# Optimization experiments

Measured on AMD Instinct MI355X. Metric: run time of the kernel, lower is better.

The kernel has to match this reference:

```python
import jax, jax.numpy as jnp
import numpy as np

N, D = 8192, 128
NOISEVAR = 1.0

def _softplusinverse(v):
    return np.log(1.0 - np.exp(-v)) + v

def setup_inputs() -> dict:
    key = jax.random.key(0)
    kx, kn = jax.random.split(key)
    x = jax.random.normal(kx, (N, D), dtype=jnp.float32)
    noise = jax.random.normal(kn, (N, D), dtype=jnp.float32)
    phi = jnp.asarray(_softplusinverse(NOISEVAR), dtype=jnp.float32)
    return {"x": x, "phi": phi, "noise": noise}

def reference(x, phi, noise):
    # x: [n, d] encoded features; phi: scalar noise param; noise: [n, d] i.i.d. N(0,1)
    n = x.shape[0]
    var = jax.nn.softplus(phi)
    # Pairwise squared L2 distances via Gram-matrix trick (same math as
    # norm(x_i - x_j)^2, avoids the [n, n, d] broadcast intermediate).
    sq = jnp.sum(x * x, axis=1)                                  # [n]
    d2 = jnp.maximum(sq[:, None] + sq[None, :] - 2.0 * (x @ x.T), 0.0)  # [n, n]
    kde_contribution = jnp.mean(jax.nn.logsumexp(-0.5 * d2 / var, axis=1))
    IXT_nats = jnp.log(jnp.float32(n)) - kde_contribution
    IXT = IXT_nats / jnp.log(jnp.float32(2.0))  # bits=True -> nats2bits
    out = x + var * noise                        # training=True noise injection
    return out, IXT
```

## Files before the change

kernel.cpp:

```cpp
#include <hip/hip_runtime.h>

#define N 8192
#define D 128
#define T64 64
#define NT64 (N / T64)

typedef __attribute__((ext_vector_type(4))) int intx4;
typedef unsigned long long u64;

static __device__ inline float softplus_of(const float* __restrict__ phi) {
    float p = phi[0];
    return (p > 20.f) ? p : log1pf(__expf(p));
}


__global__ __launch_bounds__(256) void k1_quant(
        const float* __restrict__ x,
        signed char* __restrict__ q8, int* __restrict__ sqv,
        float* __restrict__ rowsum) {
    int gid = blockIdx.x * 256 + threadIdx.x;
    int row = gid >> 4;
    int gc  = gid & 15;

    const float* xs = x + (size_t)row * D + gc * 8;
    float4 u = *(const float4*)xs, v = *(const float4*)(xs + 4);

    float f[8] = {u.x, u.y, u.z, u.w, v.x, v.y, v.z, v.w};
    u64 pack = 0;
    int s = 0;
    #pragma unroll
    for (int k = 0; k < 8; k++) {
        float c = fminf(fmaxf(f[k] * 16.f, -127.f), 127.f);
        int q = (int)rintf(c);
        s += q * q;
        pack |= ((u64)(q & 255)) << (8 * k);
    }
    *(u64*)&q8[(size_t)row * D + gc * 8] = pack;

    #pragma unroll
    for (int m = 1; m < 16; m <<= 1) s += __shfl_xor(s, m, 64);
    if (gc == 0) { sqv[row] = s; rowsum[row] = 0.f; }
}

__global__ __launch_bounds__(256, 3) void k2_gram(
        const signed char* __restrict__ q8, const float* __restrict__ phi,
        const int* __restrict__ sqv, float* __restrict__ rowsum) {
    const int w    = blockIdx.x * 4 + (threadIdx.x >> 6);
    const int lane = threadIdx.x & 63;
    const int lrow = lane & 15;
    const int quad = lane >> 4;

    const int cnt = (w < 2112) ? 3 : 2;
    int start     = (w < 2112) ? 3 * w : 2 * w + 2112;
    int ti = 0, rem = start, len = NT64;
    while (rem >= len) { rem -= len; ++ti; --len; }
    int tj = ti + rem;

    float var = softplus_of(phi);
    const float c2 = ((-0.5f / var) * 1.4426950408889634f) * (1.f / 256.f);
    const int Ts = (int)ceilf(30.f / (-c2));

    intx4 af[4][2], bf[4][2];
    int   sqi[4][4];
    int curTi = -1;

    #pragma unroll
    for (int nt = 0; nt < 4; nt++) {
        const signed char* br = q8 + (size_t)(tj * T64 + nt * 16 + lrow) * D + quad * 16;
        bf[nt][0] = *(const intx4*)br;
        bf[nt][1] = *(const intx4*)(br + 64);
    }

    for (int r = 0; r < cnt; ++r) {
        const int iB = ti * T64, jB = tj * T64;

        int sje[4];
        #pragma unroll
        for (int nt = 0; nt < 4; nt++)
            sje[nt] = sqv[jB + nt * 16 + lrow];

        if (ti != curTi) {
            #pragma unroll
            for (int mt = 0; mt < 4; mt++) {
                const signed char* ar =
                    q8 + (size_t)(iB + mt * 16 + lrow) * D + quad * 16;
                af[mt][0] = *(const intx4*)ar;
                af[mt][1] = *(const intx4*)(ar + 64);
            }
            #pragma unroll
            for (int mt = 0; mt < 4; mt++)
                #pragma unroll
                for (int reg = 0; reg < 4; reg++)
                    sqi[mt][reg] = sqv[iB + mt * 16 + quad * 4 + reg];
            curTi = ti;
        }

        int nti = ti, ntj = tj + 1;
        if (ntj == NT64) { ++nti; ntj = nti; }
        const bool more = (r + 1 < cnt);

        #pragma unroll
        for (int nt = 0; nt < 4; nt++) {
            intx4 acc[4] = {};
            #pragma unroll
            for (int kk = 0; kk < 2; kk++)
                #pragma unroll
                for (int mt = 0; mt < 4; mt++)
                    acc[mt] = __builtin_amdgcn_mfma_i32_16x16x64_i8(
                        af[mt][kk], bf[nt][kk], acc[mt], 0, 0, 0);

            if (more) {
                const signed char* br =
                    q8 + (size_t)(ntj * T64 + nt * 16 + lrow) * D + quad * 16;
                bf[nt][0] = *(const intx4*)br;
                bf[nt][1] = *(const intx4*)(br + 64);
            }

            const int sj = sje[nt];
            int mn = 0x7fffffff;
            #pragma unroll
            for (int mt = 0; mt < 4; mt++)
                #pragma unroll
                for (int reg = 0; reg < 4; reg++) {
                    int d2s = sqi[mt][reg] + sj - (acc[mt][reg] << 1);
                    mn = min(mn, d2s);
                }

            if (__any(mn < Ts)) {
                float colv = 0.f;
                #pragma unroll
                for (int mt = 0; mt < 4; mt++)
                    #pragma unroll
                    for (int reg = 0; reg < 4; reg++) {
                        int d2s = sqi[mt][reg] + sj - (acc[mt][reg] << 1);
                        float p = __builtin_amdgcn_exp2f((float)d2s * c2);
                        colv += p;
                        float rv = p;
                        rv += __shfl_xor(rv, 1, 64);
                        rv += __shfl_xor(rv, 2, 64);
                        rv += __shfl_xor(rv, 4, 64);
                        rv += __shfl_xor(rv, 8, 64);
                        if (lrow == 0)
                            atomicAdd(&rowsum[iB + mt * 16 + quad * 4 + reg], rv);
                    }
                if (ti != tj) {
                    colv += __shfl_xor(colv, 16, 64);
                    colv += __shfl_xor(colv, 32, 64);
                    if (quad == 0)
                        atomicAdd(&rowsum[jB + nt * 16 + lrow], colv);
                }
            }
        }

        ti = nti; tj = ntj;
    }
}

__global__ __launch_bounds__(1024) void k3_final(
        const float* __restrict__ rowsum, float* __restrict__ out_ixt) {
    __shared__ float red[16];
    int t = threadIdx.x;
    float local = 0.f;
    for (int i = t; i < N; i += 1024) local += logf(rowsum[i]);
    #pragma unroll
    for (int m = 1; m < 64; m <<= 1) local += __shfl_xor(local, m, 64);
    if ((t & 63) == 0) red[t >> 6] = local;
    __syncthreads();
    if (t < 16) {
        float v = red[t];
        #pragma unroll
        for (int m = 1; m < 16; m <<= 1) v += __shfl_xor(v, m, 64);
        if (t == 0) {
            float kde = v / (float)N;
            out_ixt[0] = (logf((float)N) - kde) * 1.4426950408889634f;
        }
    }
}

__global__ __launch_bounds__(256) void k4_out(
        const float* __restrict__ x, const float* __restrict__ phi,
        const float* __restrict__ noise, float* __restrict__ out) {
    int gid = blockIdx.x * 256 + threadIdx.x;
    float var = softplus_of(phi);
    const float* xs = x     + (size_t)gid * 8;
    const float* ns = noise + (size_t)gid * 8;
    float4 u  = *(const float4*)xs, v  = *(const float4*)(xs + 4);
    float4 nu = *(const float4*)ns, nv = *(const float4*)(ns + 4);
    float4 o0, o1;
    o0.x = u.x + var * nu.x; o0.y = u.y + var * nu.y;
    o0.z = u.z + var * nu.z; o0.w = u.w + var * nu.w;
    o1.x = v.x + var * nv.x; o1.y = v.y + var * nv.y;
    o1.z = v.z + var * nv.z; o1.w = v.w + var * nv.w;
    float* od = out + (size_t)gid * 8;
    *(float4*)od = o0; *(float4*)(od + 4) = o1;
}

extern "C" void kernel_launch(void* const* d_in, const int* in_sizes, int n_in,
                              void* d_out, int out_size, void* d_ws, size_t ws_size,
                              hipStream_t stream) {
    const float* x     = (const float*)d_in[0];
    const float* phi   = (const float*)d_in[1];
    const float* noise = (const float*)d_in[2];
    float* out = (float*)d_out;

    signed char* q8  = (signed char*)out;
    int*   sqv    = (int*)(out + (size_t)N * D / 4);
    float* rowsum = (float*)(sqv + N);

    k1_quant<<<(N * 16) / 256, 256, 0, stream>>>(x, q8, sqv, rowsum);
    k2_gram<<<768, 256, 0, stream>>>(q8, phi, sqv, rowsum);
    k3_final<<<1, 1024, 0, stream>>>(rowsum, out + (size_t)N * D);
    k4_out<<<(N * D / 8) / 256, 256, 0, stream>>>(x, phi, noise, out);
}
```

Measured before the change: 93.60 us.

## Fuse quantize, gram, reduction and output into one cooperative kernel

Replaces the four separate launches with a single cooperative kernel of 512 blocks that uses grid-wide syncs between the quantize, tiled int8 Gram/logsumexp, log-reduction and noise-output phases. Work per wave in the Gram phase is rebalanced to 4-5 tile pairs to fit the smaller persistent grid, and the final reduction becomes atomics plus a last-phase finalize. The aim is to remove launch gaps and the single-block final kernel, at the cost of grid-sync overhead and lower occupancy (launch bounds 256,2). It falls back to the old multi-kernel path if the cooperative launch fails.

```diff
diff --git a/kernel.cpp b/kernel.cpp
--- a/kernel.cpp
+++ b/kernel.cpp
@@ -1,9 +1,13 @@
 #include <hip/hip_runtime.h>
+#include <hip/hip_cooperative_groups.h>
+
+namespace cg = cooperative_groups;
 
 #define N 8192
 #define D 128
 #define T64 64
 #define NT64 (N / T64)
+#define GBLK 512
 
 typedef __attribute__((ext_vector_type(4))) int intx4;
 typedef unsigned long long u64;
@@ -13,6 +17,179 @@
     return (p > 20.f) ? p : log1pf(__expf(p));
 }
 
+__global__ __launch_bounds__(256, 2) void fused(
+        const float* __restrict__ x, const float* __restrict__ phi,
+        const float* __restrict__ noise, float* out) {
+    signed char* q8   = (signed char*)out;
+    int*         sqv    = (int*)(out + (size_t)N * D / 4);
+    float*       rowsum = (float*)(sqv + N);
+    float*       ixt    = out + (size_t)N * D;
+
+    cg::grid_group grid = cg::this_grid();
+    const int tid = threadIdx.x;
+    const int gid = blockIdx.x * 256 + tid;
+    const float var = softplus_of(phi);
+
+    {
+        int row = gid >> 4, gc = gid & 15;
+        const float* xs = x + (size_t)row * D + gc * 8;
+        float4 u = *(const float4*)xs, v = *(const float4*)(xs + 4);
+        float f[8] = {u.x, u.y, u.z, u.w, v.x, v.y, v.z, v.w};
+        u64 pack = 0;
+        int s = 0;
+        #pragma unroll
+        for (int k = 0; k < 8; k++) {
+            float c = fminf(fmaxf(f[k] * 16.f, -127.f), 127.f);
+            int q = (int)rintf(c);
+            s += q * q;
+            pack |= ((u64)(q & 255)) << (8 * k);
+        }
+        *(u64*)&q8[(size_t)row * D + gc * 8] = pack;
+        #pragma unroll
+        for (int m = 1; m < 16; m <<= 1) s += __shfl_xor(s, m, 64);
+        if (gc == 0) { sqv[row] = s; rowsum[row] = 0.f; }
+        if (gid == 0) ixt[0] = 0.f;
+    }
+    grid.sync();
+
+    {
+        const int w    = blockIdx.x * 4 + (tid >> 6);
+        const int lane = tid & 63;
+        const int lrow = lane & 15;
+        const int quad = lane >> 4;
+
+        const int cnt = (w < 64) ? 5 : 4;
+        int start     = (w < 64) ? 5 * w : 4 * w + 64;
+        int ti = 0, rem = start, len = NT64;
+        while (rem >= len) { rem -= len; ++ti; --len; }
+        int tj = ti + rem;
+
+        const float c2 = ((-0.5f / var) * 1.4426950408889634f) * (1.f / 256.f);
+        const int Ts = (int)ceilf(30.f / (-c2));
+
+        intx4 af[4][2], bf[4][2];
+        int   sqi[4][4];
+        int curTi = -1;
+
+        #pragma unroll
+        for (int nt = 0; nt < 4; nt++) {
+            const signed char* br = q8 + (size_t)(tj * T64 + nt * 16 + lrow) * D + quad * 16;
+            bf[nt][0] = *(const intx4*)br;
+            bf[nt][1] = *(const intx4*)(br + 64);
+        }
+
+        for (int r = 0; r < cnt; ++r) {
+            const int iB = ti * T64, jB = tj * T64;
+
+            int sje[4];
+            #pragma unroll
+            for (int nt = 0; nt < 4; nt++)
+                sje[nt] = sqv[jB + nt * 16 + lrow];
+
+            if (ti != curTi) {
+                #pragma unroll
+                for (int mt = 0; mt < 4; mt++) {
+                    const signed char* ar =
+                        q8 + (size_t)(iB + mt * 16 + lrow) * D + quad * 16;
+                    af[mt][0] = *(const intx4*)ar;
+                    af[mt][1] = *(const intx4*)(ar + 64);
+                }
+                #pragma unroll
+                for (int mt = 0; mt < 4; mt++)
+                    #pragma unroll
+                    for (int reg = 0; reg < 4; reg++)
+                        sqi[mt][reg] = sqv[iB + mt * 16 + quad * 4 + reg];
+                curTi = ti;
+            }
+
+            int nti = ti, ntj = tj + 1;
+            if (ntj == NT64) { ++nti; ntj = nti; }
+            const bool more = (r + 1 < cnt);
+
+            #pragma unroll
+            for (int nt = 0; nt < 4; nt++) {
+                intx4 acc[4] = {};
+                #pragma unroll
+                for (int kk = 0; kk < 2; kk++)
+                    #pragma unroll
+                    for (int mt = 0; mt < 4; mt++)
+                        acc[mt] = __builtin_amdgcn_mfma_i32_16x16x64_i8(
+                            af[mt][kk], bf[nt][kk], acc[mt], 0, 0, 0);
+
+                if (more) {
+                    const signed char* br =
+                        q8 + (size_t)(ntj * T64 + nt * 16 + lrow) * D + quad * 16;
+                    bf[nt][0] = *(const intx4*)br;
+                    bf[nt][1] = *(const intx4*)(br + 64);
+                }
+
+                const int sj = sje[nt];
+                int mn = 0x7fffffff;
+                #pragma unroll
+                for (int mt = 0; mt < 4; mt++)
+                    #pragma unroll
+                    for (int reg = 0; reg < 4; reg++) {
+                        int d2s = sqi[mt][reg] + sj - (acc[mt][reg] << 1);
+                        mn = min(mn, d2s);
+                    }
+
+                if (__any(mn < Ts)) {
+                    float colv = 0.f;
+                    #pragma unroll
+                    for (int mt = 0; mt < 4; mt++)
+                        #pragma unroll
+                        for (int reg = 0; reg < 4; reg++) {
+                            int d2s = sqi[mt][reg] + sj - (acc[mt][reg] << 1);
+                            float p = __builtin_amdgcn_exp2f((float)d2s * c2);
+                            colv += p;
+                            float rv = p;
+                            rv += __shfl_xor(rv, 1, 64);
+                            rv += __shfl_xor(rv, 2, 64);
+                            rv += __shfl_xor(rv, 4, 64);
+                            rv += __shfl_xor(rv, 8, 64);
+                            if (lrow == 0)
+                                atomicAdd(&rowsum[iB + mt * 16 + quad * 4 + reg], rv);
+                        }
+                    if (ti != tj) {
+                        colv += __shfl_xor(colv, 16, 64);
+                        colv += __shfl_xor(colv, 32, 64);
+                        if (quad == 0)
+                            atomicAdd(&rowsum[jB + nt * 16 + lrow], colv);
+                    }
+                }
+            }
+
+            ti = nti; tj = ntj;
+        }
+    }
+    grid.sync();
+
+    if (gid < N) {
+        float l = logf(rowsum[gid]);
+        #pragma unroll
+        for (int m = 1; m < 64; m <<= 1) l += __shfl_xor(l, m, 64);
+        if ((tid & 63) == 0) atomicAdd(ixt, l);
+    }
+    grid.sync();
+
+    {
+        const float* xs = x     + (size_t)gid * 8;
+        const float* ns = noise + (size_t)gid * 8;
+        float4 u  = *(const float4*)xs, v  = *(const float4*)(xs + 4);
+        float4 nu = *(const float4*)ns, nv = *(const float4*)(ns + 4);
+        float4 o0, o1;
+        o0.x = u.x + var * nu.x; o0.y = u.y + var * nu.y;
+        o0.z = u.z + var * nu.z; o0.w = u.w + var * nu.w;
+        o1.x = v.x + var * nv.x; o1.y = v.y + var * nv.y;
+        o1.z = v.z + var * nv.z; o1.w = v.w + var * nv.w;
+        if (gid == 0) {
+            float S = ixt[0];
+            ixt[0] = (logf((float)N) - S / (float)N) * 1.4426950408889634f;
+        }
+        float* od = out + (size_t)gid * 8;
+        *(float4*)od = o0; *(float4*)(od + 4) = o1;
+    }
+}
 
 __global__ __launch_bounds__(256) void k1_quant(
         const float* __restrict__ x,
@@ -21,10 +198,8 @@
     int gid = blockIdx.x * 256 + threadIdx.x;
     int row = gid >> 4;
     int gc  = gid & 15;
-
     const float* xs = x + (size_t)row * D + gc * 8;
     float4 u = *(const float4*)xs, v = *(const float4*)(xs + 4);
-
     float f[8] = {u.x, u.y, u.z, u.w, v.x, v.y, v.z, v.w};
     u64 pack = 0;
     int s = 0;
@@ -36,7 +211,6 @@
         pack |= ((u64)(q & 255)) << (8 * k);
     }
     *(u64*)&q8[(size_t)row * D + gc * 8] = pack;
-
     #pragma unroll
     for (int m = 1; m < 16; m <<= 1) s += __shfl_xor(s, m, 64);
     if (gc == 0) { sqv[row] = s; rowsum[row] = 0.f; }
@@ -49,36 +223,29 @@
     const int lane = threadIdx.x & 63;
     const int lrow = lane & 15;
     const int quad = lane >> 4;
-
     const int cnt = (w < 2112) ? 3 : 2;
     int start     = (w < 2112) ? 3 * w : 2 * w + 2112;
     int ti = 0, rem = start, len = NT64;
     while (rem >= len) { rem -= len; ++ti; --len; }
     int tj = ti + rem;
-
     float var = softplus_of(phi);
     const float c2 = ((-0.5f / var) * 1.4426950408889634f) * (1.f / 256.f);
     const int Ts = (int)ceilf(30.f / (-c2));
-
     intx4 af[4][2], bf[4][2];
     int   sqi[4][4];
     int curTi = -1;
-
     #pragma unroll
     for (int nt = 0; nt < 4; nt++) {
         const signed char* br = q8 + (size_t)(tj * T64 + nt * 16 + lrow) * D + quad * 16;
         bf[nt][0] = *(const intx4*)br;
         bf[nt][1] = *(const intx4*)(br + 64);
     }
-
     for (int r = 0; r < cnt; ++r) {
         const int iB = ti * T64, jB = tj * T64;
-
         int sje[4];
         #pragma unroll
         for (int nt = 0; nt < 4; nt++)
             sje[nt] = sqv[jB + nt * 16 + lrow];
-
         if (ti != curTi) {
             #pragma unroll
             for (int mt = 0; mt < 4; mt++) {
@@ -94,11 +261,9 @@
                     sqi[mt][reg] = sqv[iB + mt * 16 + quad * 4 + reg];
             curTi = ti;
         }
-
         int nti = ti, ntj = tj + 1;
         if (ntj == NT64) { ++nti; ntj = nti; }
         const bool more = (r + 1 < cnt);
-
         #pragma unroll
         for (int nt = 0; nt < 4; nt++) {
             intx4 acc[4] = {};
@@ -108,14 +273,12 @@
                 for (int mt = 0; mt < 4; mt++)
                     acc[mt] = __builtin_amdgcn_mfma_i32_16x16x64_i8(
                         af[mt][kk], bf[nt][kk], acc[mt], 0, 0, 0);
-
             if (more) {
                 const signed char* br =
                     q8 + (size_t)(ntj * T64 + nt * 16 + lrow) * D + quad * 16;
                 bf[nt][0] = *(const intx4*)br;
                 bf[nt][1] = *(const intx4*)(br + 64);
             }
-
             const int sj = sje[nt];
             int mn = 0x7fffffff;
             #pragma unroll
@@ -125,7 +288,6 @@
                     int d2s = sqi[mt][reg] + sj - (acc[mt][reg] << 1);
                     mn = min(mn, d2s);
                 }
-
             if (__any(mn < Ts)) {
                 float colv = 0.f;
                 #pragma unroll
@@ -151,7 +313,6 @@
                 }
             }
         }
-
         ti = nti; tj = ntj;
     }
 }
@@ -203,12 +364,17 @@
     const float* noise = (const float*)d_in[2];
     float* out = (float*)d_out;
 
-    signed char* q8  = (signed char*)out;
-    int*   sqv    = (int*)(out + (size_t)N * D / 4);
-    float* rowsum = (float*)(sqv + N);
-
-    k1_quant<<<(N * 16) / 256, 256, 0, stream>>>(x, q8, sqv, rowsum);
-    k2_gram<<<768, 256, 0, stream>>>(q8, phi, sqv, rowsum);
-    k3_final<<<1, 1024, 0, stream>>>(rowsum, out + (size_t)N * D);
-    k4_out<<<(N * D / 8) / 256, 256, 0, stream>>>(x, phi, noise, out);
-}
+    void* args[] = {(void*)&x, (void*)&phi, (void*)&noise, (void*)&out};
+    hipError_t e = hipLaunchCooperativeKernel(
+        reinterpret_cast<void*>(fused), dim3(GBLK), dim3(256), args, 0, stream);
+    if (e != hipSuccess) {
+        (void)hipGetLastError();
+        signed char* q8  = (signed char*)out;
+        int*   sqv    = (int*)(out + (size_t)N * D / 4);
+        float* rowsum = (float*)(sqv + N);
+        k1_quant<<<(N * 16) / 256, 256, 0, stream>>>(x, q8, sqv, rowsum);
+        k2_gram<<<768, 256, 0, stream>>>(q8, phi, sqv, rowsum);
+        k3_final<<<1, 1024, 0, stream>>>(rowsum, out + (size_t)N * D);
+        k4_out<<<(N * D / 8) / 256, 256, 0, stream>>>(x, phi, noise, out);
+    }
+}
```

Result: slower. 256.6 us (+174.1%).

## Fuse output noise into prep, finalize in gram kernel, add cheaper tile skip test

Applied to the files above, without the earlier changes.

The noise-injection output for rows beyond the scratch prefix is now written by the quantization kernel, and the final out kernel only covers the prefix rows used as scratch. The separate logsumexp finalize kernel is folded into the gram kernel through a last-block-done atomic counter. Each 16-row group's minimum squared norm is precomputed, so the gram kernel can reject a tile using only a max over the accumulators before computing full distances. This removes one launch and some redundant x reads, at the cost of a grid-wide counter and extra scratch writes.

```diff
diff --git a/kernel.cpp b/kernel.cpp
--- a/kernel.cpp
+++ b/kernel.cpp
@@ -4,6 +4,8 @@
 #define D 128
 #define T64 64
 #define NT64 (N / T64)
+#define PREFIX 2192
+#define K2BLK 768
 
 typedef __attribute__((ext_vector_type(4))) int intx4;
 typedef unsigned long long u64;
@@ -14,11 +16,15 @@
 }
 
 
-__global__ __launch_bounds__(256) void k1_quant(
-        const float* __restrict__ x,
+__global__ __launch_bounds__(256) void k1_prep(
+        const float* __restrict__ x, const float* __restrict__ phi,
+        const float* __restrict__ noise, float* __restrict__ out,
         signed char* __restrict__ q8, int* __restrict__ sqv,
-        float* __restrict__ rowsum) {
-    int gid = blockIdx.x * 256 + threadIdx.x;
+        float* __restrict__ rowsum, int* __restrict__ sqmin16,
+        int* __restrict__ counter) {
+    __shared__ int smin[16];
+    int tid = threadIdx.x;
+    int gid = blockIdx.x * 256 + tid;
     int row = gid >> 4;
     int gc  = gid & 15;
 
@@ -39,14 +45,40 @@
 
     #pragma unroll
     for (int m = 1; m < 16; m <<= 1) s += __shfl_xor(s, m, 64);
-    if (gc == 0) { sqv[row] = s; rowsum[row] = 0.f; }
+    if (gc == 0) { sqv[row] = s; rowsum[row] = 0.f; smin[tid >> 4] = s; }
+    if (gid == 0) counter[0] = 0;
+    __syncthreads();
+    if (tid == 0) {
+        int m = smin[0];
+        #pragma unroll
+        for (int k = 1; k < 16; k++) m = min(m, smin[k]);
+        sqmin16[blockIdx.x] = m;
+    }
+
+    if (row >= PREFIX) {
+        float var = softplus_of(phi);
+        const float* ns = noise + (size_t)row * D + gc * 8;
+        float4 nu = *(const float4*)ns, nv = *(const float4*)(ns + 4);
+        float4 o0, o1;
+        o0.x = u.x + var * nu.x; o0.y = u.y + var * nu.y;
+        o0.z = u.z + var * nu.z; o0.w = u.w + var * nu.w;
+        o1.x = v.x + var * nv.x; o1.y = v.y + var * nv.y;
+        o1.z = v.z + var * nv.z; o1.w = v.w + var * nv.w;
+        float* od = out + (size_t)row * D + gc * 8;
+        *(float4*)od = o0; *(float4*)(od + 4) = o1;
+    }
 }
 
 __global__ __launch_bounds__(256, 3) void k2_gram(
         const signed char* __restrict__ q8, const float* __restrict__ phi,
-        const int* __restrict__ sqv, float* __restrict__ rowsum) {
-    const int w    = blockIdx.x * 4 + (threadIdx.x >> 6);
-    const int lane = threadIdx.x & 63;
+        const int* __restrict__ sqv, float* __restrict__ rowsum,
+        const int* __restrict__ sqmin16, int* __restrict__ counter,
+        float* __restrict__ out_ixt) {
+    __shared__ float red[4];
+    __shared__ int sh_last;
+    const int tid  = threadIdx.x;
+    const int w    = blockIdx.x * 4 + (tid >> 6);
+    const int lane = tid & 63;
     const int lrow = lane & 15;
     const int quad = lane >> 4;
 
@@ -62,6 +94,7 @@
 
     intx4 af[4][2], bf[4][2];
     int   sqi[4][4];
+    int   sqiMin = 0;
     int curTi = -1;
 
     #pragma unroll
@@ -74,10 +107,12 @@
     for (int r = 0; r < cnt; ++r) {
         const int iB = ti * T64, jB = tj * T64;
 
-        int sje[4];
-        #pragma unroll
-        for (int nt = 0; nt < 4; nt++)
+        int sje[4], sjm[4];
+        #pragma unroll
+        for (int nt = 0; nt < 4; nt++) {
             sje[nt] = sqv[jB + nt * 16 + lrow];
+            sjm[nt] = sqmin16[tj * 4 + nt];
+        }
 
         if (ti != curTi) {
             #pragma unroll
@@ -92,6 +127,8 @@
                 #pragma unroll
                 for (int reg = 0; reg < 4; reg++)
                     sqi[mt][reg] = sqv[iB + mt * 16 + quad * 4 + reg];
+            sqiMin = min(min(sqmin16[ti * 4 + 0], sqmin16[ti * 4 + 1]),
+                         min(sqmin16[ti * 4 + 2], sqmin16[ti * 4 + 3]));
             curTi = ti;
         }
 
@@ -116,62 +153,77 @@
                 bf[nt][1] = *(const intx4*)(br + 64);
             }
 
-            const int sj = sje[nt];
-            int mn = 0x7fffffff;
+            int mx = acc[0][0];
             #pragma unroll
             for (int mt = 0; mt < 4; mt++)
                 #pragma unroll
-                for (int reg = 0; reg < 4; reg++) {
-                    int d2s = sqi[mt][reg] + sj - (acc[mt][reg] << 1);
-                    mn = min(mn, d2s);
-                }
-
-            if (__any(mn < Ts)) {
-                float colv = 0.f;
+                for (int reg = 0; reg < 4; reg++)
+                    mx = max(mx, acc[mt][reg]);
+            const int Sthr = sqiMin + sjm[nt] - Ts;
+
+            if (__any((mx << 1) > Sthr)) {
+                const int sj = sje[nt];
+                int mn = 0x7fffffff;
                 #pragma unroll
                 for (int mt = 0; mt < 4; mt++)
                     #pragma unroll
                     for (int reg = 0; reg < 4; reg++) {
                         int d2s = sqi[mt][reg] + sj - (acc[mt][reg] << 1);
-                        float p = __builtin_amdgcn_exp2f((float)d2s * c2);
-                        colv += p;
-                        float rv = p;
-                        rv += __shfl_xor(rv, 1, 64);
-                        rv += __shfl_xor(rv, 2, 64);
-                        rv += __shfl_xor(rv, 4, 64);
-                        rv += __shfl_xor(rv, 8, 64);
-                        if (lrow == 0)
-                            atomicAdd(&rowsum[iB + mt * 16 + quad * 4 + reg], rv);
+                        mn = min(mn, d2s);
                     }
-                if (ti != tj) {
-                    colv += __shfl_xor(colv, 16, 64);
-                    colv += __shfl_xor(colv, 32, 64);
-                    if (quad == 0)
-                        atomicAdd(&rowsum[jB + nt * 16 + lrow], colv);
+
+                if (__any(mn < Ts)) {
+                    float colv = 0.f;
+                    #pragma unroll
+                    for (int mt = 0; mt < 4; mt++)
+                        #pragma unroll
+                        for (int reg = 0; reg < 4; reg++) {
+                            int d2s = sqi[mt][reg] + sj - (acc[mt][reg] << 1);
+                            float p = __builtin_amdgcn_exp2f((float)d2s * c2);
+                            colv += p;
+                            float rv = p;
+                            rv += __shfl_xor(rv, 1, 64);
+                            rv += __shfl_xor(rv, 2, 64);
+                            rv += __shfl_xor(rv, 4, 64);
+                            rv += __shfl_xor(rv, 8, 64);
+                            if (lrow == 0)
+                                atomicAdd(&rowsum[iB + mt * 16 + quad * 4 + reg], rv);
+                        }
+                    if (ti != tj) {
+                        colv += __shfl_xor(colv, 16, 64);
+                        colv += __shfl_xor(colv, 32, 64);
+                        if (quad == 0)
+                            atomicAdd(&rowsum[jB + nt * 16 + lrow], colv);
+                    }
                 }
             }
         }
 
         ti = nti; tj = ntj;
     }
-}
-
-__global__ __launch_bounds__(1024) void k3_final(
-        const float* __restrict__ rowsum, float* __restrict__ out_ixt) {
-    __shared__ float red[16];
-    int t = threadIdx.x;
-    float local = 0.f;
-    for (int i = t; i < N; i += 1024) local += logf(rowsum[i]);
-    #pragma unroll
-    for (int m = 1; m < 64; m <<= 1) local += __shfl_xor(local, m, 64);
-    if ((t & 63) == 0) red[t >> 6] = local;
+
     __syncthreads();
-    if (t < 16) {
-        float v = red[t];
-        #pragma unroll
-        for (int m = 1; m < 16; m <<= 1) v += __shfl_xor(v, m, 64);
-        if (t == 0) {
-            float kde = v / (float)N;
+    if (tid == 0) {
+        __threadfence();
+        int old = __hip_atomic_fetch_add(counter, 1, __ATOMIC_ACQ_REL,
+                                         __HIP_MEMORY_SCOPE_AGENT);
+        sh_last = (old == K2BLK - 1);
+    }
+    __syncthreads();
+    if (sh_last) {
+        float l = 0.f;
+        for (int i = tid; i < N; i += 256) {
+            float rv = __hip_atomic_load(&rowsum[i], __ATOMIC_RELAXED,
+                                         __HIP_MEMORY_SCOPE_AGENT);
+            l += logf(rv);
+        }
+        #pragma unroll
+        for (int m = 1; m < 64; m <<= 1) l += __shfl_xor(l, m, 64);
+        if ((tid & 63) == 0) red[tid >> 6] = l;
+        __syncthreads();
+        if (tid == 0) {
+            float S = red[0] + red[1] + red[2] + red[3];
+            float kde = S / (float)N;
             out_ixt[0] = (logf((float)N) - kde) * 1.4426950408889634f;
         }
     }
@@ -203,12 +255,15 @@
     const float* noise = (const float*)d_in[2];
     float* out = (float*)d_out;
 
-    signed char* q8  = (signed char*)out;
-    int*   sqv    = (int*)(out + (size_t)N * D / 4);
-    float* rowsum = (float*)(sqv + N);
-
-    k1_quant<<<(N * 16) / 256, 256, 0, stream>>>(x, q8, sqv, rowsum);
-    k2_gram<<<768, 256, 0, stream>>>(q8, phi, sqv, rowsum);
-    k3_final<<<1, 1024, 0, stream>>>(rowsum, out + (size_t)N * D);
-    k4_out<<<(N * D / 8) / 256, 256, 0, stream>>>(x, phi, noise, out);
-}
+    signed char* q8     = (signed char*)out;
+    int*         sqv     = (int*)(out + (size_t)N * D / 4);
+    float*       rowsum  = (float*)(sqv + N);
+    int*         sqmin16 = (int*)(rowsum + N);
+    int*         counter = sqmin16 + (N / 16);
+
+    k1_prep<<<(N * 16) / 256, 256, 0, stream>>>(
+        x, phi, noise, out, q8, sqv, rowsum, sqmin16, counter);
+    k2_gram<<<K2BLK, 256, 0, stream>>>(
+        q8, phi, sqv, rowsum, sqmin16, counter, out + (size_t)N * D);
+    k4_out<<<(PREFIX * 16) / 256, 256, 0, stream>>>(x, phi, noise, out);
+}
```

Measured after the change: 111.8 us. +19.5%, slower.

## Fuse noise output into quant pass, one tile per wave, merge final reduction

Applied to the files above, without the earlier changes.

The quantisation kernel now also writes x + var*noise for rows at or above 2176, which lie past the scratch region held in the output buffer. The final output kernel writes the remaining rows and, in its first block, also does the logsumexp reduction, so the separate reduce launch goes away. The Gram kernel gives each wave a single 64x64 tile pair, found with a closed-form triangular index, instead of looping over 2-3 tiles, and raises the launch-bounds occupancy hint from 3 to 4. The aim is to cut launches and the duplicate reads of x, at the cost of losing B-fragment prefetch reuse across tiles and launching more waves.

```diff
diff --git a/kernel.cpp b/kernel.cpp
--- a/kernel.cpp
+++ b/kernel.cpp
@@ -4,6 +4,9 @@
 #define D 128
 #define T64 64
 #define NT64 (N / T64)
+#define NPAIR (NT64 * (NT64 + 1) / 2)
+#define PREFIX 2176
+#define TBASE(t) ((t) * NT64 - ((t) * ((t) - 1)) / 2)
 
 typedef __attribute__((ext_vector_type(4))) int intx4;
 typedef unsigned long long u64;
@@ -14,11 +17,13 @@
 }
 
 
-__global__ __launch_bounds__(256) void k1_quant(
-        const float* __restrict__ x,
+__global__ __launch_bounds__(256) void k1_prep(
+        const float* __restrict__ x, const float* __restrict__ phi,
+        const float* __restrict__ noise, float* __restrict__ out,
         signed char* __restrict__ q8, int* __restrict__ sqv,
         float* __restrict__ rowsum) {
-    int gid = blockIdx.x * 256 + threadIdx.x;
+    int tid = threadIdx.x;
+    int gid = blockIdx.x * 256 + tid;
     int row = gid >> 4;
     int gc  = gid & 15;
 
@@ -40,159 +45,163 @@
     #pragma unroll
     for (int m = 1; m < 16; m <<= 1) s += __shfl_xor(s, m, 64);
     if (gc == 0) { sqv[row] = s; rowsum[row] = 0.f; }
-}
-
-__global__ __launch_bounds__(256, 3) void k2_gram(
+
+    if (row >= PREFIX) {
+        float var = softplus_of(phi);
+        const float* ns = noise + (size_t)row * D + gc * 8;
+        float4 nu = *(const float4*)ns, nv = *(const float4*)(ns + 4);
+        float4 o0, o1;
+        o0.x = u.x + var * nu.x; o0.y = u.y + var * nu.y;
+        o0.z = u.z + var * nu.z; o0.w = u.w + var * nu.w;
+        o1.x = v.x + var * nv.x; o1.y = v.y + var * nv.y;
+        o1.z = v.z + var * nv.z; o1.w = v.w + var * nv.w;
+        float* od = out + (size_t)row * D + gc * 8;
+        *(float4*)od = o0; *(float4*)(od + 4) = o1;
+    }
+}
+
+__global__ __launch_bounds__(256, 4) void k2_gram(
         const signed char* __restrict__ q8, const float* __restrict__ phi,
         const int* __restrict__ sqv, float* __restrict__ rowsum) {
-    const int w    = blockIdx.x * 4 + (threadIdx.x >> 6);
-    const int lane = threadIdx.x & 63;
+    const int tid  = threadIdx.x;
+    const int w    = blockIdx.x * 4 + (tid >> 6);
+    const int lane = tid & 63;
     const int lrow = lane & 15;
     const int quad = lane >> 4;
 
-    const int cnt = (w < 2112) ? 3 : 2;
-    int start     = (w < 2112) ? 3 * w : 2 * w + 2112;
-    int ti = 0, rem = start, len = NT64;
-    while (rem >= len) { rem -= len; ++ti; --len; }
-    int tj = ti + rem;
-
-    float var = softplus_of(phi);
+    const float fm = (float)(2 * NT64 + 1);
+    int ti = (int)((fm - sqrtf(fm * fm - 8.0f * (float)w)) * 0.5f);
+    while (TBASE(ti + 1) <= w) ++ti;
+    while (TBASE(ti) > w) --ti;
+    const int tj = ti + (w - TBASE(ti));
+
+    const float var = softplus_of(phi);
     const float c2 = ((-0.5f / var) * 1.4426950408889634f) * (1.f / 256.f);
     const int Ts = (int)ceilf(30.f / (-c2));
 
-    intx4 af[4][2], bf[4][2];
-    int   sqi[4][4];
-    int curTi = -1;
-
+    const int iB = ti * T64, jB = tj * T64;
+
+    intx4 af[4][2], bf[4][2], sqi[4];
+    int   sje[4];
+    #pragma unroll
+    for (int mt = 0; mt < 4; mt++) {
+        const signed char* ar = q8 + (size_t)(iB + mt * 16 + lrow) * D + quad * 16;
+        af[mt][0] = *(const intx4*)ar;
+        af[mt][1] = *(const intx4*)(ar + 64);
+    }
     #pragma unroll
     for (int nt = 0; nt < 4; nt++) {
-        const signed char* br = q8 + (size_t)(tj * T64 + nt * 16 + lrow) * D + quad * 16;
+        const signed char* br = q8 + (size_t)(jB + nt * 16 + lrow) * D + quad * 16;
         bf[nt][0] = *(const intx4*)br;
         bf[nt][1] = *(const intx4*)(br + 64);
     }
-
-    for (int r = 0; r < cnt; ++r) {
-        const int iB = ti * T64, jB = tj * T64;
-
-        int sje[4];
-        #pragma unroll
-        for (int nt = 0; nt < 4; nt++)
-            sje[nt] = sqv[jB + nt * 16 + lrow];
-
-        if (ti != curTi) {
-            #pragma unroll
-            for (int mt = 0; mt < 4; mt++) {
-                const signed char* ar =
-                    q8 + (size_t)(iB + mt * 16 + lrow) * D + quad * 16;
-                af[mt][0] = *(const intx4*)ar;
-                af[mt][1] = *(const intx4*)(ar + 64);
-            }
+    #pragma unroll
+    for (int mt = 0; mt < 4; mt++)
+        sqi[mt] = *(const intx4*)&sqv[iB + mt * 16 + quad * 4];
+    #pragma unroll
+    for (int nt = 0; nt < 4; nt++)
+        sje[nt] = sqv[jB + nt * 16 + lrow];
+
+    #pragma unroll
+    for (int nt = 0; nt < 4; nt++) {
+        intx4 acc[4] = {};
+        #pragma unroll
+        for (int kk = 0; kk < 2; kk++)
             #pragma unroll
             for (int mt = 0; mt < 4; mt++)
-                #pragma unroll
-                for (int reg = 0; reg < 4; reg++)
-                    sqi[mt][reg] = sqv[iB + mt * 16 + quad * 4 + reg];
-            curTi = ti;
-        }
-
-        int nti = ti, ntj = tj + 1;
-        if (ntj == NT64) { ++nti; ntj = nti; }
-        const bool more = (r + 1 < cnt);
-
-        #pragma unroll
-        for (int nt = 0; nt < 4; nt++) {
-            intx4 acc[4] = {};
+                acc[mt] = __builtin_amdgcn_mfma_i32_16x16x64_i8(
+                    af[mt][kk], bf[nt][kk], acc[mt], 0, 0, 0);
+
+        const int sj = sje[nt];
+        int mn = 0x7fffffff;
+        #pragma unroll
+        for (int mt = 0; mt < 4; mt++)
             #pragma unroll
-            for (int kk = 0; kk < 2; kk++)
-                #pragma unroll
-                for (int mt = 0; mt < 4; mt++)
-                    acc[mt] = __builtin_amdgcn_mfma_i32_16x16x64_i8(
-                        af[mt][kk], bf[nt][kk], acc[mt], 0, 0, 0);
-
-            if (more) {
-                const signed char* br =
-                    q8 + (size_t)(ntj * T64 + nt * 16 + lrow) * D + quad * 16;
-                bf[nt][0] = *(const intx4*)br;
-                bf[nt][1] = *(const intx4*)(br + 64);
+            for (int reg = 0; reg < 4; reg++) {
+                int d2s = sqi[mt][reg] + sj - (acc[mt][reg] << 1);
+                mn = min(mn, d2s);
             }
 
-            const int sj = sje[nt];
-            int mn = 0x7fffffff;
+        if (__any(mn < Ts)) {
+            float colv = 0.f;
             #pragma unroll
             for (int mt = 0; mt < 4; mt++)
                 #pragma unroll
                 for (int reg = 0; reg < 4; reg++) {
                     int d2s = sqi[mt][reg] + sj - (acc[mt][reg] << 1);
-                    mn = min(mn, d2s);
+                    float p = __builtin_amdgcn_exp2f((float)d2s * c2);
+                    colv += p;
+                    float rv = p;
+                    rv += __shfl_xor(rv, 1, 64);
+                    rv += __shfl_xor(rv, 2, 64);
+                    rv += __shfl_xor(rv, 4, 64);
+                    rv += __shfl_xor(rv, 8, 64);
+                    if (lrow == 0)
+                        atomicAdd(&rowsum[iB + mt * 16 + quad * 4 + reg], rv);
                 }
-
-            if (__any(mn < Ts)) {
-                float colv = 0.f;
-                #pragma unroll
-                for (int mt = 0; mt < 4; mt++)
-                    #pragma unroll
-                    for (int reg = 0; reg < 4; reg++) {
-                        int d2s = sqi[mt][reg] + sj - (acc[mt][reg] << 1);
-                        float p = __builtin_amdgcn_exp2f((float)d2s * c2);
-                        colv += p;
-                        float rv = p;
-                        rv += __shfl_xor(rv, 1, 64);
-                        rv += __shfl_xor(rv, 2, 64);
-                        rv += __shfl_xor(rv, 4, 64);
-                        rv += __shfl_xor(rv, 8, 64);
-                        if (lrow == 0)
-                            atomicAdd(&rowsum[iB + mt * 16 + quad * 4 + reg], rv);
-                    }
-                if (ti != tj) {
-                    colv += __shfl_xor(colv, 16, 64);
-                    colv += __shfl_xor(colv, 32, 64);
-                    if (quad == 0)
-                        atomicAdd(&rowsum[jB + nt * 16 + lrow], colv);
-                }
+            if (ti != tj) {
+                colv += __shfl_xor(colv, 16, 64);
+                colv += __shfl_xor(colv, 32, 64);
+                if (quad == 0)
+                    atomicAdd(&rowsum[jB + nt * 16 + lrow], colv);
             }
         }
-
-        ti = nti; tj = ntj;
-    }
-}
-
-__global__ __launch_bounds__(1024) void k3_final(
-        const float* __restrict__ rowsum, float* __restrict__ out_ixt) {
-    __shared__ float red[16];
-    int t = threadIdx.x;
-    float local = 0.f;
-    for (int i = t; i < N; i += 1024) local += logf(rowsum[i]);
-    #pragma unroll
-    for (int m = 1; m < 64; m <<= 1) local += __shfl_xor(local, m, 64);
-    if ((t & 63) == 0) red[t >> 6] = local;
-    __syncthreads();
-    if (t < 16) {
-        float v = red[t];
-        #pragma unroll
-        for (int m = 1; m < 16; m <<= 1) v += __shfl_xor(v, m, 64);
-        if (t == 0) {
-            float kde = v / (float)N;
-            out_ixt[0] = (logf((float)N) - kde) * 1.4426950408889634f;
-        }
     }
 }
 
 __global__ __launch_bounds__(256) void k4_out(
         const float* __restrict__ x, const float* __restrict__ phi,
-        const float* __restrict__ noise, float* __restrict__ out) {
-    int gid = blockIdx.x * 256 + threadIdx.x;
-    float var = softplus_of(phi);
-    const float* xs = x     + (size_t)gid * 8;
-    const float* ns = noise + (size_t)gid * 8;
-    float4 u  = *(const float4*)xs, v  = *(const float4*)(xs + 4);
-    float4 nu = *(const float4*)ns, nv = *(const float4*)(ns + 4);
-    float4 o0, o1;
-    o0.x = u.x + var * nu.x; o0.y = u.y + var * nu.y;
-    o0.z = u.z + var * nu.z; o0.w = u.w + var * nu.w;
-    o1.x = v.x + var * nv.x; o1.y = v.y + var * nv.y;
-    o1.z = v.z + var * nv.z; o1.w = v.w + var * nv.w;
-    float* od = out + (size_t)gid * 8;
-    *(float4*)od = o0; *(float4*)(od + 4) = o1;
+        const float* __restrict__ noise, float* out,
+        const float* __restrict__ rowsum) {
+    const int tid = threadIdx.x;
+    const float var = softplus_of(phi);
+
+    if (blockIdx.x == 0) {
+        __shared__ float red[4];
+        float l = 0.f;
+        #pragma unroll 4
+        for (int i = tid; i < N; i += 256) l += logf(rowsum[i]);
+        #pragma unroll
+        for (int m = 1; m < 64; m <<= 1) l += __shfl_xor(l, m, 64);
+        if ((tid & 63) == 0) red[tid >> 6] = l;
+        __syncthreads();
+        if (tid == 0) {
+            float S = red[0] + red[1] + red[2] + red[3];
+            float kde = S / (float)N;
+            out[(size_t)N * D] =
+                (logf((float)N) - kde) * 1.4426950408889634f;
+        }
+        __syncthreads();
+        #pragma unroll
+        for (int it = 0; it < 4; it++) {
+            int idx = it * 256 + tid;
+            size_t off = (size_t)2112 * D + idx * 8;
+            const float* xs = x + off;
+            const float* ns = noise + off;
+            float4 u  = *(const float4*)xs, v  = *(const float4*)(xs + 4);
+            float4 nu = *(const float4*)ns, nv = *(const float4*)(ns + 4);
+            float4 o0, o1;
+            o0.x = u.x + var * nu.x; o0.y = u.y + var * nu.y;
+            o0.z = u.z + var * nu.z; o0.w = u.w + var * nu.w;
+            o1.x = v.x + var * nv.x; o1.y = v.y + var * nv.y;
+            o1.z = v.z + var * nv.z; o1.w = v.w + var * nv.w;
+            float* od = out + off;
+            *(float4*)od = o0; *(float4*)(od + 4) = o1;
+        }
+    } else {
+        size_t gid = (size_t)(blockIdx.x - 1) * 256 + tid;
+        const float* xs = x     + gid * 8;
+        const float* ns = noise + gid * 8;
+        float4 u  = *(const float4*)xs, v  = *(const float4*)(xs + 4);
+        float4 nu = *(const float4*)ns, nv = *(const float4*)(ns + 4);
+        float4 o0, o1;
+        o0.x = u.x + var * nu.x; o0.y = u.y + var * nu.y;
+        o0.z = u.z + var * nu.z; o0.w = u.w + var * nu.w;
+        o1.x = v.x + var * nv.x; o1.y = v.y + var * nv.y;
+        o1.z = v.z + var * nv.z; o1.w = v.w + var * nv.w;
+        float* od = out + gid * 8;
+        *(float4*)od = o0; *(float4*)(od + 4) = o1;
+    }
 }
 
 extern "C" void kernel_launch(void* const* d_in, const int* in_sizes, int n_in,
@@ -203,12 +212,13 @@
     const float* noise = (const float*)d_in[2];
     float* out = (float*)d_out;
 
-    signed char* q8  = (signed char*)out;
-    int*   sqv    = (int*)(out + (size_t)N * D / 4);
-    float* rowsum = (float*)(sqv + N);
-
-    k1_quant<<<(N * 16) / 256, 256, 0, stream>>>(x, q8, sqv, rowsum);
-    k2_gram<<<768, 256, 0, stream>>>(q8, phi, sqv, rowsum);
-    k3_final<<<1, 1024, 0, stream>>>(rowsum, out + (size_t)N * D);
-    k4_out<<<(N * D / 8) / 256, 256, 0, stream>>>(x, phi, noise, out);
-}
+    signed char* q8     = (signed char*)out;
+    int*         sqv    = (int*)(out + (size_t)N * D / 4);
+    float*       rowsum = (float*)(sqv + N);
+
+    k1_prep<<<(N * 16) / 256, 256, 0, stream>>>(
+        x, phi, noise, out, q8, sqv, rowsum);
+    k2_gram<<<NPAIR / 4, 256, 0, stream>>>(q8, phi, sqv, rowsum);
+    k4_out<<<1 + (2112 * 16) / 256, 256, 0, stream>>>(
+        x, phi, noise, out, rowsum);
+}
```

After: 98.22 us. 4.9% more time.
